# Performance work log

Measured on AMD Instinct MI355X. Metric: run time of the kernel, lower is better.

## Reference

```python
import jax, jax.numpy as jnp
import numpy as np

NEG_SLOPE = 0.2  # PyG GATConv default negative_slope


def gat_layer(x, src, dst, W, a_src, a_dst, bias, concat, N):
    """PyG GATConv: h = xW; e_ij = LeakyReLU(a_src.h_j + a_dst.h_i);
    alpha = segment-softmax over incoming edges of i; out_i = sum_j alpha_ij h_j."""
    H, C = a_src.shape
    h = (x @ W).reshape(N, H, C)                      # [N,H,C]
    alpha_s = jnp.einsum('nhc,hc->nh', h, a_src)      # [N,H]
    alpha_d = jnp.einsum('nhc,hc->nh', h, a_dst)      # [N,H]
    e = jax.nn.leaky_relu(alpha_s[src] + alpha_d[dst], NEG_SLOPE)  # [E,H]
    # numerically-stable segment softmax over destination nodes
    m = jax.ops.segment_max(e, dst, num_segments=N)   # [N,H]
    e = jnp.exp(e - m[dst])
    denom = jax.ops.segment_sum(e, dst, num_segments=N)
    alpha = e / (denom[dst] + 1e-16)                  # [E,H]
    msg = h[src] * alpha[:, :, None]                  # [E,H,C]
    out = jax.ops.segment_sum(msg, dst, num_segments=N)  # [N,H,C]
    out = out.reshape(N, H * C) if concat else out.mean(axis=1)
    return out + bias


def setup_inputs() -> dict:
    key = jax.random.key(0)
    ks = jax.random.split(key, 12)
    N, E, F_IN, C, H = 50000, 800000, 512, 32, 8
    s = 0.05
    x = jax.random.normal(ks[0], (N, F_IN), dtype=jnp.float32)
    edge_index = jax.random.randint(ks[1], (2, E), 0, N, dtype=jnp.int64)
    W1 = jax.random.normal(ks[2], (F_IN, H * C), dtype=jnp.float32) * s
    as1 = jax.random.normal(ks[3], (H, C), dtype=jnp.float32) * s
    ad1 = jax.random.normal(ks[4], (H, C), dtype=jnp.float32) * s
    b1 = jnp.zeros((H * C,), dtype=jnp.float32)
    W2 = jax.random.normal(ks[5], (H * C, H * C), dtype=jnp.float32) * s
    as2 = jax.random.normal(ks[6], (H, C), dtype=jnp.float32) * s
    ad2 = jax.random.normal(ks[7], (H, C), dtype=jnp.float32) * s
    b2 = jnp.zeros((C,), dtype=jnp.float32)
    Wp = jax.random.normal(ks[8], (C, 1), dtype=jnp.float32) * s
    bp = jnp.zeros((1,), dtype=jnp.float32)
    return {"edge_index": edge_index, "x": x, "W1": W1, "as1": as1, "ad1": ad1,
            "b1": b1, "W2": W2, "as2": as2, "ad2": ad2, "b2": b2,
            "Wp": Wp, "bp": bp}


def reference(edge_index, x, W1, as1, ad1, b1, W2, as2, ad2, b2, Wp, bp):
    N = x.shape[0]
    # PyG GATConv adds self-loops by default
    loops = jnp.arange(N, dtype=edge_index.dtype)
    src = jnp.concatenate([edge_index[0], loops])
    dst = jnp.concatenate([edge_index[1], loops])
    h = gat_layer(x, src, dst, W1, as1, ad1, b1, concat=True, N=N)
    h = jax.nn.relu(h)
    # F.dropout(training=self.training) is identity in eval mode
    h = gat_layer(h, src, dst, W2, as2, ad2, b2, concat=False, N=N)
    return jax.nn.sigmoid(h @ Wp + bp)   # [N,1]
```

## Files before the change

### kernel.cpp

```cpp
#include <hip/hip_runtime.h>
#include <math.h>

#define H_HEADS 8
#define C_DIM   32
#define HC      256
#define F_IN    512
#define NEG_SLOPE 0.2f

typedef __attribute__((ext_vector_type(8))) short    bf16x8;
typedef __attribute__((ext_vector_type(4))) short    s16x4;
typedef __attribute__((ext_vector_type(4))) float    f32x4;
typedef __attribute__((ext_vector_type(2))) float    f32x2;
typedef __attribute__((ext_vector_type(8))) _Float16 h16x8;

__device__ __forceinline__ short f2bf(float f) {
    union { float f; unsigned u; } v; v.f = f;
    unsigned r = v.u + 0x7FFF + ((v.u >> 16) & 1);
    return (short)(r >> 16);
}

__device__ __forceinline__ void gl2lds16(const short* g, short* l) {
    __builtin_amdgcn_global_load_lds(
        (const __attribute__((address_space(1))) void*)g,
        (__attribute__((address_space(3))) void*)l, 16, 0, 0);
}

__global__ void wfrag_kernel(const float* __restrict__ W, short* __restrict__ Wf, int K)
{
    int tid = blockIdx.x * 256 + threadIdx.x;
    if (tid >= K * HC) return;
    int j  = tid & 7;
    int l  = (tid >> 3) & 63;
    int nb = (tid >> 9) & 15;
    int s  = tid >> 13;
    int k  = s * 32 + (l >> 4) * 8 + j;
    int n  = nb * 16 + (l & 15);
    Wf[tid] = f2bf(W[(size_t)k * HC + n]);
}

template<bool ABF16>
__global__ __launch_bounds__(256) void gemm_mfma(const void* __restrict__ Aptr,
    const short* __restrict__ Bf, unsigned char* __restrict__ h8,
    const float* __restrict__ a_s, const float* __restrict__ a_d,
    float* __restrict__ alpha_s, float* __restrict__ alpha_d, int M, int K)
{
    __shared__ short Bs[2][8192];
    __shared__ float Als[512], Ald[512];

    const int tid  = threadIdx.x;
    const int w    = tid >> 6;
    const int lane = tid & 63;
    const int quad = lane >> 4;
    const int ml   = lane & 15;
    const int bm   = blockIdx.x * 64;

    const int rowA = bm + w * 16 + ml;
    const int rowL = rowA < M ? rowA : M - 1;

    f32x4 acc[16];
    #pragma unroll
    for (int nb = 0; nb < 16; ++nb) acc[nb] = (f32x4){0.f, 0.f, 0.f, 0.f};

    const float* A32 = (const float*)Aptr;
    const short* A16 = (const short*)Aptr;
    const int nsteps = K >> 5;

    {
        const short* g = Bf + (size_t)w * 2048 + lane * 8;
        short* l = &Bs[0][w * 2048];
        #pragma unroll
        for (int c = 0; c < 4; ++c) gl2lds16(g + c * 512, l + c * 512);
    }

    float4 p0, p1;
    bf16x8 pb;
    if (ABF16) {
        pb = *(const bf16x8*)(A16 + (size_t)rowL * K + quad * 8);
    } else {
        const float* ap = A32 + (size_t)rowL * K + quad * 8;
        p0 = *(const float4*)(ap);
        p1 = *(const float4*)(ap + 4);
    }

    for (int s = 0; s < nsteps; ++s) {
        __syncthreads();

        if (s + 1 < nsteps) {
            const short* g = Bf + (size_t)(s + 1) * 8192 + w * 2048 + lane * 8;
            short* l = &Bs[(s + 1) & 1][w * 2048];
            #pragma unroll
            for (int c = 0; c < 4; ++c) gl2lds16(g + c * 512, l + c * 512);
        }

        bf16x8 af;
        if (ABF16) {
            af = pb;
            if (s + 1 < nsteps)
                pb = *(const bf16x8*)(A16 + (size_t)rowL * K + (s + 1) * 32 + quad * 8);
        } else {
            af[0] = f2bf(p0.x); af[1] = f2bf(p0.y); af[2] = f2bf(p0.z); af[3] = f2bf(p0.w);
            af[4] = f2bf(p1.x); af[5] = f2bf(p1.y); af[6] = f2bf(p1.z); af[7] = f2bf(p1.w);
            if (s + 1 < nsteps) {
                const float* ap = A32 + (size_t)rowL * K + (s + 1) * 32 + quad * 8;
                p0 = *(const float4*)(ap);
                p1 = *(const float4*)(ap + 4);
            }
        }

        const short* bsrc = &Bs[s & 1][lane * 8];
        #pragma unroll
        for (int nb = 0; nb < 16; ++nb) {
            bf16x8 bfr = *(const bf16x8*)(bsrc + nb * 512);
            acc[nb] = __builtin_amdgcn_mfma_f32_16x16x32_bf16(af, bfr, acc[nb], 0, 0, 0);
        }
    }

    float as_v[16], ad_v[16];
    #pragma unroll
    for (int nb = 0; nb < 16; ++nb) {
        as_v[nb] = a_s[nb * 16 + ml];
        ad_v[nb] = a_d[nb * 16 + ml];
    }

    #pragma unroll
    for (int r = 0; r < 4; ++r) {
        const int rl  = w * 16 + quad * 4 + r;
        const int row = bm + rl;

        if (row < M) {
            unsigned char* hrow = h8 + (size_t)row * HC;
            #pragma unroll
            for (int i = 0; i < 8; ++i) {
                int pk = __builtin_amdgcn_cvt_pk_fp8_f32(acc[2 * i][r], acc[2 * i + 1][r], 0, false);
                hrow[(2 * i) * 16 + ml]     = (unsigned char)(pk & 0xFF);
                hrow[(2 * i + 1) * 16 + ml] = (unsigned char)((pk >> 8) & 0xFF);
            }
        }

        float hs[8], hd[8];
        #pragma unroll
        for (int q = 0; q < 8; ++q) {
            hs[q] = acc[2 * q][r] * as_v[2 * q] + acc[2 * q + 1][r] * as_v[2 * q + 1];
            hd[q] = acc[2 * q][r] * ad_v[2 * q] + acc[2 * q + 1][r] * ad_v[2 * q + 1];
        }
        #pragma unroll
        for (int off = 1; off < 16; off <<= 1) {
            #pragma unroll
            for (int q = 0; q < 8; ++q) {
                hs[q] += __shfl_xor(hs[q], off);
                hd[q] += __shfl_xor(hd[q], off);
            }
        }
        if (ml == 0) {
            #pragma unroll
            for (int q = 0; q < 8; ++q) {
                Als[rl * 8 + q] = hs[q];
                Ald[rl * 8 + q] = hd[q];
            }
        }
    }
    __syncthreads();
    #pragma unroll
    for (int k = 0; k < 2; ++k) {
        int idx = tid + k * 256;
        int rl = idx >> 3, q = idx & 7;
        int row = bm + rl;
        if (row < M) {
            alpha_s[(size_t)row * H_HEADS + q] = Als[idx];
            alpha_d[(size_t)row * H_HEADS + q] = Ald[idx];
        }
    }
}

__global__ __launch_bounds__(256) void wcalc_kernel(const int2* __restrict__ es,
    const float* __restrict__ alpha_s, const float* __restrict__ alpha_d,
    _Float16* __restrict__ wq, int P)
{
    int p = blockIdx.x * 256 + threadIdx.x;
    if (p >= P) return;
    int2 sd = es[p];
    const float4* as = (const float4*)(alpha_s + (size_t)sd.x * H_HEADS);
    const float4* ad = (const float4*)(alpha_d + (size_t)sd.y * H_HEADS);
    float4 s0 = as[0], s1 = as[1], d0 = ad[0], d1 = ad[1];
    float e[8] = {s0.x + d0.x, s0.y + d0.y, s0.z + d0.z, s0.w + d0.w,
                  s1.x + d1.x, s1.y + d1.y, s1.z + d1.z, s1.w + d1.w};
    h16x8 o;
    #pragma unroll
    for (int h = 0; h < 8; ++h) {
        float v = e[h] > 0.f ? e[h] : NEG_SLOPE * e[h];
        o[h] = (_Float16)__expf(v);
    }
    *(h16x8*)(wq + (size_t)p * H_HEADS) = o;
}

__global__ void zero_int(int* __restrict__ p, int n)
{
    int i = blockIdx.x * 256 + threadIdx.x;
    if (i < n) p[i] = 0;
}

__global__ void hist_kernel(const int* __restrict__ ei, int E, int N,
                            int* __restrict__ cnt)
{
    int e = blockIdx.x * 256 + threadIdx.x;
    if (e < E) atomicAdd(&cnt[ei[E + e]], 1);
    else if (e < E + N) atomicAdd(&cnt[e - E], 1);
}

__global__ __launch_bounds__(256) void scan_sum(const int* __restrict__ cnt, int n,
                                                int* __restrict__ chunk_sum)
{
    __shared__ int lds[256];
    int b = blockIdx.x, t = threadIdx.x;
    int base = b * 1024 + t * 4;
    int s = 0;
    #pragma unroll
    for (int j = 0; j < 4; ++j) { int i = base + j; if (i < n) s += cnt[i]; }
    lds[t] = s; __syncthreads();
    for (int off = 128; off > 0; off >>= 1) {
        if (t < off) lds[t] += lds[t + off];
        __syncthreads();
    }
    if (t == 0) chunk_sum[b] = lds[0];
}

__global__ __launch_bounds__(256) void scan_local(const int* __restrict__ cnt, int n,
    const int* __restrict__ chunk_sum, int nch, int* __restrict__ row_ptr)
{
    __shared__ int lds[256];
    int b = blockIdx.x, t = threadIdx.x;
    int lane = t & 63;

    int cs  = (lane < nch) ? chunk_sum[lane] : 0;
    int pre = (lane < b)   ? cs : 0;
    int tot = cs;
    #pragma unroll
    for (int off = 32; off > 0; off >>= 1) {
        pre += __shfl_xor(pre, off);
        tot += __shfl_xor(tot, off);
    }

    int base = b * 1024 + t * 4;
    int v[4]; int s = 0;
    #pragma unroll
    for (int j = 0; j < 4; ++j) { int i = base + j; v[j] = (i < n) ? cnt[i] : 0; s += v[j]; }
    lds[t] = s; __syncthreads();
    for (int off = 1; off < 256; off <<= 1) {
        int u = (t >= off) ? lds[t - off] : 0;
        __syncthreads();
        lds[t] += u;
        __syncthreads();
    }
    int run = lds[t] - s + pre;
    #pragma unroll
    for (int j = 0; j < 4; ++j) {
        int i = base + j;
        if (i < n) row_ptr[i] = run;
        run += v[j];
    }
    if (b == gridDim.x - 1 && t == 0) row_ptr[n] = tot;
}

__global__ void scatter_kernel(const int* __restrict__ ei, int E, int N,
    const int* __restrict__ row_ptr, int* __restrict__ cnt, int2* __restrict__ es)
{
    int e = blockIdx.x * 256 + threadIdx.x;
    int src, dst;
    if (e < E)          { src = ei[e]; dst = ei[E + e]; }
    else if (e < E + N) { src = dst = e - E; }
    else return;
    int pos = row_ptr[dst] + atomicSub(&cnt[dst], 1) - 1;
    es[pos] = make_int2(src, dst);
}

#define ACC4(word, wgt, base_) do { \
    f32x2 lo_ = __builtin_amdgcn_cvt_pk_f32_fp8((word), false); \
    f32x2 hi_ = __builtin_amdgcn_cvt_pk_f32_fp8((word), true);  \
    acc[(base_) + 0] = fmaf((wgt), lo_[0], acc[(base_) + 0]); \
    acc[(base_) + 1] = fmaf((wgt), lo_[1], acc[(base_) + 1]); \
    acc[(base_) + 2] = fmaf((wgt), hi_[0], acc[(base_) + 2]); \
    acc[(base_) + 3] = fmaf((wgt), hi_[1], acc[(base_) + 3]); \
} while (0)

__global__ __launch_bounds__(256) void agg1_kernel(const unsigned char* __restrict__ h8,
    const _Float16* __restrict__ wq, const int* __restrict__ row_ptr,
    const int2* __restrict__ es, const float* __restrict__ bias,
    short* __restrict__ z_bf, int N)
{
    const int l  = threadIdx.x & 63;
    const int i  = blockIdx.x * 4 + (threadIdx.x >> 6);
    if (i >= N) return;
    const int c  = l & 15;
    const int eo = l >> 4;
    const int hh = c >> 1;
    const int beg = row_ptr[i], end = row_ptr[i + 1];

    float acc[16];
    #pragma unroll
    for (int j = 0; j < 16; ++j) acc[j] = 0.f;
    float dsum = 0.f;

    int p = beg;
    for (; p + 7 < end; p += 8) {
        int p0 = p + eo, p1 = p + 4 + eo;
        int s0 = es[p0].x, s1 = es[p1].x;
        float w0 = (float)wq[(size_t)p0 * 8 + hh];
        float w1 = (float)wq[(size_t)p1 * 8 + hh];
        uint4 h0 = *(const uint4*)(h8 + (size_t)s0 * 256 + c * 16);
        uint4 h1 = *(const uint4*)(h8 + (size_t)s1 * 256 + c * 16);
        ACC4(h0.x, w0, 0); ACC4(h0.y, w0, 4); ACC4(h0.z, w0, 8); ACC4(h0.w, w0, 12);
        ACC4(h1.x, w1, 0); ACC4(h1.y, w1, 4); ACC4(h1.z, w1, 8); ACC4(h1.w, w1, 12);
        dsum += w0 + w1;
    }
    for (; p < end; p += 4) {
        int pe = p + eo;
        int pc = pe < end ? pe : end - 1;
        int s0 = es[pc].x;
        float w0 = pe < end ? (float)wq[(size_t)pc * 8 + hh] : 0.f;
        uint4 h0 = *(const uint4*)(h8 + (size_t)s0 * 256 + c * 16);
        ACC4(h0.x, w0, 0); ACC4(h0.y, w0, 4); ACC4(h0.z, w0, 8); ACC4(h0.w, w0, 12);
        dsum += w0;
    }

    #pragma unroll
    for (int j = 0; j < 16; ++j) {
        acc[j] += __shfl_xor(acc[j], 32);
        acc[j] += __shfl_xor(acc[j], 16);
    }
    dsum += __shfl_xor(dsum, 32);
    dsum += __shfl_xor(dsum, 16);

    float inv = 1.f / (dsum + 1e-16f);
    if (eo == 0) {
        union { short s[16]; bf16x8 v[2]; } zz;
        #pragma unroll
        for (int j = 0; j < 16; ++j) {
            float z = acc[j] * inv + bias[c * 16 + j];
            zz.s[j] = f2bf(z > 0.f ? z : 0.f);
        }
        *(bf16x8*)(z_bf + (size_t)i * HC + c * 16)     = zz.v[0];
        *(bf16x8*)(z_bf + (size_t)i * HC + c * 16 + 8) = zz.v[1];
    }
}

__global__ __launch_bounds__(256) void agg2_kernel(const unsigned char* __restrict__ h8,
    const _Float16* __restrict__ wq, const int* __restrict__ row_ptr,
    const int2* __restrict__ es, const float* __restrict__ b2,
    const float* __restrict__ Wp, const float* __restrict__ bp,
    float* __restrict__ out, int N)
{
    const int l  = threadIdx.x & 63;
    const int i  = blockIdx.x * 4 + (threadIdx.x >> 6);
    if (i >= N) return;
    const int c  = l & 15;
    const int eo = l >> 4;
    const int hh = c >> 1;
    const int beg = row_ptr[i], end = row_ptr[i + 1];

    float acc[16];
    #pragma unroll
    for (int j = 0; j < 16; ++j) acc[j] = 0.f;
    float dsum = 0.f;

    int p = beg;
    for (; p + 7 < end; p += 8) {
        int p0 = p + eo, p1 = p + 4 + eo;
        int s0 = es[p0].x, s1 = es[p1].x;
        float w0 = (float)wq[(size_t)p0 * 8 + hh];
        float w1 = (float)wq[(size_t)p1 * 8 + hh];
        uint4 h0 = *(const uint4*)(h8 + (size_t)s0 * 256 + c * 16);
        uint4 h1 = *(const uint4*)(h8 + (size_t)s1 * 256 + c * 16);
        ACC4(h0.x, w0, 0); ACC4(h0.y, w0, 4); ACC4(h0.z, w0, 8); ACC4(h0.w, w0, 12);
        ACC4(h1.x, w1, 0); ACC4(h1.y, w1, 4); ACC4(h1.z, w1, 8); ACC4(h1.w, w1, 12);
        dsum += w0 + w1;
    }
    for (; p < end; p += 4) {
        int pe = p + eo;
        int pc = pe < end ? pe : end - 1;
        int s0 = es[pc].x;
        float w0 = pe < end ? (float)wq[(size_t)pc * 8 + hh] : 0.f;
        uint4 h0 = *(const uint4*)(h8 + (size_t)s0 * 256 + c * 16);
        ACC4(h0.x, w0, 0); ACC4(h0.y, w0, 4); ACC4(h0.z, w0, 8); ACC4(h0.w, w0, 12);
        dsum += w0;
    }

    #pragma unroll
    for (int j = 0; j < 16; ++j) {
        acc[j] += __shfl_xor(acc[j], 32);
        acc[j] += __shfl_xor(acc[j], 16);
    }
    dsum += __shfl_xor(dsum, 32);
    dsum += __shfl_xor(dsum, 16);

    float inv = 1.f / (dsum + 1e-16f);
    const int wb = (c & 1) << 4;
    float partial = 0.f;
    #pragma unroll
    for (int j = 0; j < 16; ++j) partial = fmaf(acc[j] * inv, Wp[wb + j], partial);
    if (eo == 0 && c < 2) {
        #pragma unroll
        for (int j = 0; j < 16; ++j) partial += 8.f * b2[c * 16 + j] * Wp[c * 16 + j];
    }
    #pragma unroll
    for (int off = 8; off > 0; off >>= 1) partial += __shfl_xor(partial, off);
    if (l == 0) out[i] = 1.f / (1.f + __expf(-(0.125f * partial + bp[0])));
}

extern "C" void kernel_launch(void* const* d_in, const int* in_sizes, int n_in,
                              void* d_out, int out_size, void* d_ws, size_t ws_size,
                              hipStream_t stream)
{
    const int*   ei  = (const int*)d_in[0];
    const float* x   = (const float*)d_in[1];
    const float* W1  = (const float*)d_in[2];
    const float* as1 = (const float*)d_in[3];
    const float* ad1 = (const float*)d_in[4];
    const float* b1  = (const float*)d_in[5];
    const float* W2  = (const float*)d_in[6];
    const float* as2 = (const float*)d_in[7];
    const float* ad2 = (const float*)d_in[8];
    const float* b2  = (const float*)d_in[9];
    const float* Wp  = (const float*)d_in[10];
    const float* bp  = (const float*)d_in[11];
    float* out = (float*)d_out;

    const int E = in_sizes[0] / 2;
    const int N = in_sizes[1] / F_IN;
    const int ET = E + N;

    float*         asb = (float*)d_ws;
    float*         adb = asb + (size_t)N * H_HEADS;
    unsigned char* h8  = (unsigned char*)(adb + (size_t)N * H_HEADS);
    short*         z1b = (short*)(h8 + (size_t)N * HC);
    short*         Wf1 = z1b + (size_t)N * HC;
    short*         Wf2 = Wf1 + (size_t)F_IN * HC;
    _Float16*      wq  = (_Float16*)(Wf2 + (size_t)HC * HC);
    int2*          es  = (int2*)(wq + (size_t)ET * H_HEADS);
    int* cnt       = (int*)(es + ET);
    int* row_ptr   = cnt + N;
    int* chunk_sum = row_ptr + N + 1;

    const int NCH = (N + 1023) / 1024;
    const int MB  = (N + 63) / 64;
    const int NB4 = (N + 3) / 4;

    zero_int<<<(N + 255) / 256, 256, 0, stream>>>(cnt, N);
    hist_kernel<<<(ET + 255) / 256, 256, 0, stream>>>(ei, E, N, cnt);
    scan_sum<<<NCH, 256, 0, stream>>>(cnt, N, chunk_sum);
    scan_local<<<NCH, 256, 0, stream>>>(cnt, N, chunk_sum, NCH, row_ptr);
    scatter_kernel<<<(ET + 255) / 256, 256, 0, stream>>>(ei, E, N, row_ptr, cnt, es);

    wfrag_kernel<<<(F_IN * HC + 255) / 256, 256, 0, stream>>>(W1, Wf1, F_IN);
    wfrag_kernel<<<(HC * HC + 255) / 256, 256, 0, stream>>>(W2, Wf2, HC);

    gemm_mfma<false><<<MB, 256, 0, stream>>>(x, Wf1, h8, as1, ad1, asb, adb, N, F_IN);
    wcalc_kernel<<<(ET + 255) / 256, 256, 0, stream>>>(es, asb, adb, wq, ET);
    agg1_kernel<<<NB4, 256, 0, stream>>>(h8, wq, row_ptr, es, b1, z1b, N);

    gemm_mfma<true><<<MB, 256, 0, stream>>>(z1b, Wf2, h8, as2, ad2, asb, adb, N, HC);
    wcalc_kernel<<<(ET + 255) / 256, 256, 0, stream>>>(es, asb, adb, wq, ET);
    agg2_kernel<<<NB4, 256, 0, stream>>>(h8, wq, row_ptr, es, b2, Wp, bp, out, N);
}
```

Before: 419.9 us.

## Fuse edge-weight computation into aggregation kernels and drop wcalc pass

```diff
diff --git a/kernel.cpp b/kernel.cpp
--- a/kernel.cpp
+++ b/kernel.cpp
@@ -11,7 +11,6 @@
 typedef __attribute__((ext_vector_type(4))) short    s16x4;
 typedef __attribute__((ext_vector_type(4))) float    f32x4;
 typedef __attribute__((ext_vector_type(2))) float    f32x2;
-typedef __attribute__((ext_vector_type(8))) _Float16 h16x8;
 
 __device__ __forceinline__ short f2bf(float f) {
     union { float f; unsigned u; } v; v.f = f;
@@ -19,23 +18,38 @@
     return (short)(r >> 16);
 }
 
+__device__ __forceinline__ bf16x8 cvt8(float4 a, float4 b) {
+    union { bf16x8 v; unsigned u[4]; } r;
+    asm("v_cvt_pk_bf16_f32 %0, %1, %2" : "=v"(r.u[0]) : "v"(a.x), "v"(a.y));
+    asm("v_cvt_pk_bf16_f32 %0, %1, %2" : "=v"(r.u[1]) : "v"(a.z), "v"(a.w));
+    asm("v_cvt_pk_bf16_f32 %0, %1, %2" : "=v"(r.u[2]) : "v"(b.x), "v"(b.y));
+    asm("v_cvt_pk_bf16_f32 %0, %1, %2" : "=v"(r.u[3]) : "v"(b.z), "v"(b.w));
+    return r.v;
+}
+
 __device__ __forceinline__ void gl2lds16(const short* g, short* l) {
     __builtin_amdgcn_global_load_lds(
         (const __attribute__((address_space(1))) void*)g,
         (__attribute__((address_space(3))) void*)l, 16, 0, 0);
 }
 
-__global__ void wfrag_kernel(const float* __restrict__ W, short* __restrict__ Wf, int K)
-{
+__global__ void wfrag_kernel(const float* __restrict__ W1, const float* __restrict__ W2,
+                             short* __restrict__ Wf1, short* __restrict__ Wf2)
+{
+    const int NW1 = F_IN * HC;
+    const int NW2 = HC * HC;
     int tid = blockIdx.x * 256 + threadIdx.x;
-    if (tid >= K * HC) return;
-    int j  = tid & 7;
-    int l  = (tid >> 3) & 63;
-    int nb = (tid >> 9) & 15;
-    int s  = tid >> 13;
+    const float* W; short* Wf; int t;
+    if (tid < NW1)            { W = W1; Wf = Wf1; t = tid; }
+    else if (tid < NW1 + NW2) { W = W2; Wf = Wf2; t = tid - NW1; }
+    else return;
+    int j  = t & 7;
+    int l  = (t >> 3) & 63;
+    int nb = (t >> 9) & 15;
+    int s  = t >> 13;
     int k  = s * 32 + (l >> 4) * 8 + j;
     int n  = nb * 16 + (l & 15);
-    Wf[tid] = f2bf(W[(size_t)k * HC + n]);
+    Wf[t] = f2bf(W[(size_t)k * HC + n]);
 }
 
 template<bool ABF16>
@@ -98,8 +112,7 @@
             if (s + 1 < nsteps)
                 pb = *(const bf16x8*)(A16 + (size_t)rowL * K + (s + 1) * 32 + quad * 8);
         } else {
-            af[0] = f2bf(p0.x); af[1] = f2bf(p0.y); af[2] = f2bf(p0.z); af[3] = f2bf(p0.w);
-            af[4] = f2bf(p1.x); af[5] = f2bf(p1.y); af[6] = f2bf(p1.z); af[7] = f2bf(p1.w);
+            af = cvt8(p0, p1);
             if (s + 1 < nsteps) {
                 const float* ap = A32 + (size_t)rowL * K + (s + 1) * 32 + quad * 8;
                 p0 = *(const float4*)(ap);
@@ -172,27 +185,6 @@
     }
 }
 
-__global__ __launch_bounds__(256) void wcalc_kernel(const int2* __restrict__ es,
-    const float* __restrict__ alpha_s, const float* __restrict__ alpha_d,
-    _Float16* __restrict__ wq, int P)
-{
-    int p = blockIdx.x * 256 + threadIdx.x;
-    if (p >= P) return;
-    int2 sd = es[p];
-    const float4* as = (const float4*)(alpha_s + (size_t)sd.x * H_HEADS);
-    const float4* ad = (const float4*)(alpha_d + (size_t)sd.y * H_HEADS);
-    float4 s0 = as[0], s1 = as[1], d0 = ad[0], d1 = ad[1];
-    float e[8] = {s0.x + d0.x, s0.y + d0.y, s0.z + d0.z, s0.w + d0.w,
-                  s1.x + d1.x, s1.y + d1.y, s1.z + d1.z, s1.w + d1.w};
-    h16x8 o;
-    #pragma unroll
-    for (int h = 0; h < 8; ++h) {
-        float v = e[h] > 0.f ? e[h] : NEG_SLOPE * e[h];
-        o[h] = (_Float16)__expf(v);
-    }
-    *(h16x8*)(wq + (size_t)p * H_HEADS) = o;
-}
-
 __global__ void zero_int(int* __restrict__ p, int n)
 {
     int i = blockIdx.x * 256 + threadIdx.x;
@@ -262,7 +254,7 @@
 }
 
 __global__ void scatter_kernel(const int* __restrict__ ei, int E, int N,
-    const int* __restrict__ row_ptr, int* __restrict__ cnt, int2* __restrict__ es)
+    const int* __restrict__ row_ptr, int* __restrict__ cnt, int* __restrict__ es)
 {
     int e = blockIdx.x * 256 + threadIdx.x;
     int src, dst;
@@ -270,7 +262,7 @@
     else if (e < E + N) { src = dst = e - E; }
     else return;
     int pos = row_ptr[dst] + atomicSub(&cnt[dst], 1) - 1;
-    es[pos] = make_int2(src, dst);
+    es[pos] = src;
 }
 
 #define ACC4(word, wgt, base_) do { \
@@ -282,10 +274,15 @@
     acc[(base_) + 3] = fmaf((wgt), hi_[1], acc[(base_) + 3]); \
 } while (0)
 
+__device__ __forceinline__ float edge_w(float av, float ad8) {
+    float e = av + ad8;
+    return __expf(e > 0.f ? e : NEG_SLOPE * e);
+}
+
 __global__ __launch_bounds__(256) void agg1_kernel(const unsigned char* __restrict__ h8,
-    const _Float16* __restrict__ wq, const int* __restrict__ row_ptr,
-    const int2* __restrict__ es, const float* __restrict__ bias,
-    short* __restrict__ z_bf, int N)
+    const float* __restrict__ asb, const float* __restrict__ adb,
+    const int* __restrict__ row_ptr, const int* __restrict__ es,
+    const float* __restrict__ bias, short* __restrict__ z_bf, int N)
 {
     const int l  = threadIdx.x & 63;
     const int i  = blockIdx.x * 4 + (threadIdx.x >> 6);
@@ -293,6 +290,7 @@
     const int c  = l & 15;
     const int eo = l >> 4;
     const int hh = c >> 1;
+    const float ad8 = adb[(size_t)i * 8 + hh];
     const int beg = row_ptr[i], end = row_ptr[i + 1];
 
     float acc[16];
@@ -302,12 +300,13 @@
 
     int p = beg;
     for (; p + 7 < end; p += 8) {
-        int p0 = p + eo, p1 = p + 4 + eo;
-        int s0 = es[p0].x, s1 = es[p1].x;
-        float w0 = (float)wq[(size_t)p0 * 8 + hh];
-        float w1 = (float)wq[(size_t)p1 * 8 + hh];
+        int s0 = es[p + eo], s1 = es[p + 4 + eo];
+        float a0 = asb[(size_t)s0 * 8 + hh];
+        float a1 = asb[(size_t)s1 * 8 + hh];
         uint4 h0 = *(const uint4*)(h8 + (size_t)s0 * 256 + c * 16);
         uint4 h1 = *(const uint4*)(h8 + (size_t)s1 * 256 + c * 16);
+        float w0 = edge_w(a0, ad8);
+        float w1 = edge_w(a1, ad8);
         ACC4(h0.x, w0, 0); ACC4(h0.y, w0, 4); ACC4(h0.z, w0, 8); ACC4(h0.w, w0, 12);
         ACC4(h1.x, w1, 0); ACC4(h1.y, w1, 4); ACC4(h1.z, w1, 8); ACC4(h1.w, w1, 12);
         dsum += w0 + w1;
@@ -315,8 +314,8 @@
     for (; p < end; p += 4) {
         int pe = p + eo;
         int pc = pe < end ? pe : end - 1;
-        int s0 = es[pc].x;
-        float w0 = pe < end ? (float)wq[(size_t)pc * 8 + hh] : 0.f;
+        int s0 = es[pc];
+        float w0 = pe < end ? edge_w(asb[(size_t)s0 * 8 + hh], ad8) : 0.f;
         uint4 h0 = *(const uint4*)(h8 + (size_t)s0 * 256 + c * 16);
         ACC4(h0.x, w0, 0); ACC4(h0.y, w0, 4); ACC4(h0.z, w0, 8); ACC4(h0.w, w0, 12);
         dsum += w0;
@@ -344,10 +343,10 @@
 }
 
 __global__ __launch_bounds__(256) void agg2_kernel(const unsigned char* __restrict__ h8,
-    const _Float16* __restrict__ wq, const int* __restrict__ row_ptr,
-    const int2* __restrict__ es, const float* __restrict__ b2,
-    const float* __restrict__ Wp, const float* __restrict__ bp,
-    float* __restrict__ out, int N)
+    const float* __restrict__ asb, const float* __restrict__ adb,
+    const int* __restrict__ row_ptr, const int* __restrict__ es,
+    const float* __restrict__ b2, const float* __restrict__ Wp,
+    const float* __restrict__ bp, float* __restrict__ out, int N)
 {
     const int l  = threadIdx.x & 63;
     const int i  = blockIdx.x * 4 + (threadIdx.x >> 6);
@@ -355,6 +354,7 @@
     const int c  = l & 15;
     const int eo = l >> 4;
     const int hh = c >> 1;
+    const float ad8 = adb[(size_t)i * 8 + hh];
     const int beg = row_ptr[i], end = row_ptr[i + 1];
 
     float acc[16];
@@ -364,12 +364,13 @@
 
     int p = beg;
     for (; p + 7 < end; p += 8) {
-        int p0 = p + eo, p1 = p + 4 + eo;
-        int s0 = es[p0].x, s1 = es[p1].x;
-        float w0 = (float)wq[(size_t)p0 * 8 + hh];
-        float w1 = (float)wq[(size_t)p1 * 8 + hh];
+        int s0 = es[p + eo], s1 = es[p + 4 + eo];
+        float a0 = asb[(size_t)s0 * 8 + hh];
+        float a1 = asb[(size_t)s1 * 8 + hh];
         uint4 h0 = *(const uint4*)(h8 + (size_t)s0 * 256 + c * 16);
         uint4 h1 = *(const uint4*)(h8 + (size_t)s1 * 256 + c * 16);
+        float w0 = edge_w(a0, ad8);
+        float w1 = edge_w(a1, ad8);
         ACC4(h0.x, w0, 0); ACC4(h0.y, w0, 4); ACC4(h0.z, w0, 8); ACC4(h0.w, w0, 12);
         ACC4(h1.x, w1, 0); ACC4(h1.y, w1, 4); ACC4(h1.z, w1, 8); ACC4(h1.w, w1, 12);
         dsum += w0 + w1;
@@ -377,8 +378,8 @@
     for (; p < end; p += 4) {
         int pe = p + eo;
         int pc = pe < end ? pe : end - 1;
-        int s0 = es[pc].x;
-        float w0 = pe < end ? (float)wq[(size_t)pc * 8 + hh] : 0.f;
+        int s0 = es[pc];
+        float w0 = pe < end ? edge_w(asb[(size_t)s0 * 8 + hh], ad8) : 0.f;
         uint4 h0 = *(const uint4*)(h8 + (size_t)s0 * 256 + c * 16);
         ACC4(h0.x, w0, 0); ACC4(h0.y, w0, 4); ACC4(h0.z, w0, 8); ACC4(h0.w, w0, 12);
         dsum += w0;
@@ -434,9 +435,8 @@
     short*         z1b = (short*)(h8 + (size_t)N * HC);
     short*         Wf1 = z1b + (size_t)N * HC;
     short*         Wf2 = Wf1 + (size_t)F_IN * HC;
-    _Float16*      wq  = (_Float16*)(Wf2 + (size_t)HC * HC);
-    int2*          es  = (int2*)(wq + (size_t)ET * H_HEADS);
-    int* cnt       = (int*)(es + ET);
+    int*           es  = (int*)(Wf2 + (size_t)HC * HC);
+    int* cnt       = es + ET;
     int* row_ptr   = cnt + N;
     int* chunk_sum = row_ptr + N + 1;
 
@@ -450,14 +450,11 @@
     scan_local<<<NCH, 256, 0, stream>>>(cnt, N, chunk_sum, NCH, row_ptr);
     scatter_kernel<<<(ET + 255) / 256, 256, 0, stream>>>(ei, E, N, row_ptr, cnt, es);
 
-    wfrag_kernel<<<(F_IN * HC + 255) / 256, 256, 0, stream>>>(W1, Wf1, F_IN);
-    wfrag_kernel<<<(HC * HC + 255) / 256, 256, 0, stream>>>(W2, Wf2, HC);
+    wfrag_kernel<<<(F_IN * HC + HC * HC + 255) / 256, 256, 0, stream>>>(W1, W2, Wf1, Wf2);
 
     gemm_mfma<false><<<MB, 256, 0, stream>>>(x, Wf1, h8, as1, ad1, asb, adb, N, F_IN);
-    wcalc_kernel<<<(ET + 255) / 256, 256, 0, stream>>>(es, asb, adb, wq, ET);
-    agg1_kernel<<<NB4, 256, 0, stream>>>(h8, wq, row_ptr, es, b1, z1b, N);
+    agg1_kernel<<<NB4, 256, 0, stream>>>(h8, asb, adb, row_ptr, es, b1, z1b, N);
 
     gemm_mfma<true><<<MB, 256, 0, stream>>>(z1b, Wf2, h8, as2, ad2, asb, adb, N, HC);
-    wcalc_kernel<<<(ET + 255) / 256, 256, 0, stream>>>(es, asb, adb, wq, ET);
-    agg2_kernel<<<NB4, 256, 0, stream>>>(h8, wq, row_ptr, es, b2, Wp, bp, out, N);
-}
+    agg2_kernel<<<NB4, 256, 0, stream>>>(h8, asb, adb, row_ptr, es, b2, Wp, bp, out, N);
+}
```

Result: faster. 404.5 us (-3.7%).
